# Optimization experiments

Hardware: AMD Instinct MI355X
Metric: run time of the kernel (lower is better)

Reference implementation:

```python
import jax, jax.numpy as jnp
import numpy as np


def setup_inputs() -> dict:
    key = jax.random.key(0)
    k1, k2 = jax.random.split(key)
    N, B, C, T = 64, 16, 22, 4000
    M = 2 * 2 * 4  # 2*m_filters*nb_classes
    xfb = jax.random.normal(k1, (N, B, C, T), dtype=jnp.float32)
    WT = jax.random.normal(k2, (B, M, C), dtype=jnp.float32) * 0.1
    return {"xfb": xfb, "WT": WT}


def reference(xfb, WT):
    # xfb: (N, B, C, T), WT: (B, M, C)
    T = xfb.shape[-1]
    x = xfb / jnp.sqrt(jnp.asarray(T, dtype=xfb.dtype))
    # Z = WT @ xfb  -> (N, B, M, T)
    Z = jnp.einsum('bmc,nbct->nbmt', WT, x)
    # diagonal of Z @ Z^T == row-wise sum of squares over T (avoid MxM Gram)
    diag = jnp.sum(Z * Z, axis=-1)          # (N, B, M)
    return jnp.log(diag / jnp.sum(diag, axis=-1, keepdims=True))
```

## Files before the change

kernel.cpp:

```cpp
#include <hip/hip_runtime.h>
#include <cmath>


#define N_ 64
#define B_ 16
#define C_ 22
#define T_ 4000
#define M_ 16

__global__ __launch_bounds__(256, 1)
void OVR_CSP_kernel(const float* __restrict__ xfb,
                    const float* __restrict__ WT,
                    float* __restrict__ out) {
    const int bid  = blockIdx.x;
    const int b    = bid & (B_ - 1);
    const int tid  = threadIdx.x;
    const int wave = tid >> 6;
    const int lane = tid & 63;

    __shared__ float dsh[M_];

    const float* __restrict__ wb = WT + b * (M_ * C_) + (4 * wave) * C_;
    float wreg[4][C_];
    #pragma unroll
    for (int j = 0; j < 4; ++j)
        #pragma unroll
        for (int c = 0; c < C_; ++c)
            wreg[j][c] = wb[j * C_ + c];

    const float* __restrict__ xb = xfb + (size_t)bid * (C_ * T_);

    float acc[4] = {0.f, 0.f, 0.f, 0.f};

    #pragma unroll 1
    for (int t = lane; t < T_; t += 64) {
        float xv[C_];
        #pragma unroll
        for (int c = 0; c < C_; ++c)
            xv[c] = xb[c * T_ + t];

        #pragma unroll
        for (int j = 0; j < 4; ++j) {
            float z = 0.f;
            #pragma unroll
            for (int c = 0; c < C_; ++c)
                z = fmaf(wreg[j][c], xv[c], z);
            acc[j] = fmaf(z, z, acc[j]);
        }
    }

    #pragma unroll
    for (int j = 0; j < 4; ++j) {
        float v = acc[j];
        #pragma unroll
        for (int off = 32; off > 0; off >>= 1)
            v += __shfl_down(v, off, 64);
        if (lane == 0) dsh[4 * wave + j] = v;
    }
    __syncthreads();

    if (tid < M_) {
        float total = 0.f;
        #pragma unroll
        for (int m = 0; m < M_; ++m) total += dsh[m];
        out[(size_t)bid * M_ + tid] = logf(dsh[tid] / total);
    }
}

extern "C" void kernel_launch(void* const* d_in, const int* in_sizes, int n_in,
                              void* d_out, int out_size, void* d_ws, size_t ws_size,
                              hipStream_t stream) {
    const float* xfb = (const float*)d_in[0];
    const float* WT  = (const float*)d_in[1];
    float* out = (float*)d_out;

    dim3 grid(N_ * B_);
    dim3 block(256);
    OVR_CSP_kernel<<<grid, block, 0, stream>>>(xfb, WT, out);
}
```

Baseline: 502.0 us.

## Stage x tiles in LDS with float4 loads shared across all four waves

Before, each of the four waves read the whole x slab from global memory with scalar loads, so every element was loaded four times. Now the block copies 256-sample tiles of x into shared memory once, using float4 global loads. Each wave then reads float4 chunks from shared memory and computes four time samples per lane. This cuts redundant global traffic and widens the loads. In exchange it adds two block barriers per tile, with no overlap between loading and compute, and a padded final tile.

New measurement: 520.3 us. 1.04x slower.

```diff
diff --git a/kernel.cpp b/kernel.cpp
--- a/kernel.cpp
+++ b/kernel.cpp
@@ -7,6 +7,8 @@
 #define C_ 22
 #define T_ 4000
 #define M_ 16
+#define TT_ 256
+#define TPAD_ 260
 
 __global__ __launch_bounds__(256, 1)
 void OVR_CSP_kernel(const float* __restrict__ xfb,
@@ -18,6 +20,7 @@
     const int wave = tid >> 6;
     const int lane = tid & 63;
 
+    __shared__ __align__(16) float xs[C_][TPAD_];
     __shared__ float dsh[M_];
 
     const float* __restrict__ wb = WT + b * (M_ * C_) + (4 * wave) * C_;
@@ -32,21 +35,45 @@
 
     float acc[4] = {0.f, 0.f, 0.f, 0.f};
 
+    const int NTILE = (T_ + TT_ - 1) / TT_;
     #pragma unroll 1
-    for (int t = lane; t < T_; t += 64) {
-        float xv[C_];
+    for (int tile = 0; tile < NTILE; ++tile) {
+        const int t0 = tile * TT_;
+
+        #pragma unroll 1
+        for (int i = tid; i < C_ * (TT_ / 4); i += 256) {
+            const int c  = i >> 6;
+            const int f4 = i & 63;
+            const int t  = t0 + 4 * f4;
+            float4 v = make_float4(0.f, 0.f, 0.f, 0.f);
+            if (t < T_) v = *(const float4*)(xb + c * T_ + t);
+            *(float4*)&xs[c][4 * f4] = v;
+        }
+        __syncthreads();
+
+        float4 z[4];
         #pragma unroll
-        for (int c = 0; c < C_; ++c)
-            xv[c] = xb[c * T_ + t];
+        for (int j = 0; j < 4; ++j) z[j] = make_float4(0.f, 0.f, 0.f, 0.f);
 
         #pragma unroll
+        for (int c = 0; c < C_; ++c) {
+            const float4 xc = *(const float4*)&xs[c][4 * lane];
+            #pragma unroll
+            for (int j = 0; j < 4; ++j) {
+                z[j].x = fmaf(wreg[j][c], xc.x, z[j].x);
+                z[j].y = fmaf(wreg[j][c], xc.y, z[j].y);
+                z[j].z = fmaf(wreg[j][c], xc.z, z[j].z);
+                z[j].w = fmaf(wreg[j][c], xc.w, z[j].w);
+            }
+        }
+        #pragma unroll
         for (int j = 0; j < 4; ++j) {
-            float z = 0.f;
-            #pragma unroll
-            for (int c = 0; c < C_; ++c)
-                z = fmaf(wreg[j][c], xv[c], z);
-            acc[j] = fmaf(z, z, acc[j]);
+            acc[j] = fmaf(z[j].x, z[j].x, acc[j]);
+            acc[j] = fmaf(z[j].y, z[j].y, acc[j]);
+            acc[j] = fmaf(z[j].z, z[j].z, acc[j]);
+            acc[j] = fmaf(z[j].w, z[j].w, acc[j]);
         }
+        __syncthreads();
     }
 
     #pragma unroll
```
